# Kernel optimization log

Hardware: AMD Instinct MI355X
Metric: run time of the kernel (lower is better)

Reference implementation:

```python
import jax, jax.numpy as jnp
import numpy as np


def setup_inputs() -> dict:
    key = jax.random.key(0)
    k1, k2, k3 = jax.random.split(key, 3)
    V, B, T = 8192, 8, 1024
    x = jax.random.randint(k1, (B, T), 0, V, dtype=jnp.int64)
    y = jax.random.randint(k2, (B, T), 0, V, dtype=jnp.int64)
    emb = jax.random.normal(k3, (V, V), dtype=jnp.float32)
    return {"x": x, "y": y, "emb": emb}


def reference(x, y, emb):
    # token embedding lookup: [B, T, C] with C == vocab_size
    logits = emb[x]
    B, T, C = logits.shape
    # Causal mean pooling. softmax over a tril(ones) mask assigns uniform
    # weight 1/(t+1) to positions 0..t, i.e. a causal running mean.
    # Equivalent to the original's avg_matrix @ logits, computed in O(T*C).
    denom = jnp.arange(1, T + 1, dtype=logits.dtype)[:, None]  # [T, 1]
    logits_prev_mean = jnp.cumsum(logits, axis=1) / denom      # [B, T, C]
    # cross_entropy with mean reduction over B*T positions
    logp = jax.nn.log_softmax(logits_prev_mean, axis=-1)
    nll = -jnp.take_along_axis(logp, y[..., None], axis=-1)[..., 0]  # [B, T]
    loss = jnp.mean(nll)
    return logits, loss
```

## Files before the change

kernel.cpp:

```cpp
#include <hip/hip_runtime.h>

#define V 8192
#define B 8
#define T 1024
#define NSEG 16
#define SEGLEN 64
#define CSLICE 1024
#define NCHUNK 32
#define CHUNK 256

typedef float f32x4 __attribute__((ext_vector_type(4)));

__device__ __forceinline__ void nt_store4(float4* p, float4 v) {
    __builtin_nontemporal_store(*(f32x4*)&v, (f32x4*)p);
}

__global__ __launch_bounds__(256) void sum_kernel(
    const float* __restrict__ emb, const int* __restrict__ x,
    float* __restrict__ segsum)
{
    const int slice = blockIdx.x;
    const int seg   = blockIdx.y;
    const int b     = blockIdx.z;
    const int lane  = threadIdx.x & 63;
    const int c4    = (slice * CSLICE + threadIdx.x * 4) >> 2;

    const int xi = x[b * T + seg * SEGLEN + lane];

    const float4* emb4 = (const float4*)emb;
    float4 acc = make_float4(0.f, 0.f, 0.f, 0.f);
    float4 vbuf[4];
#pragma unroll
    for (int k = 0; k < 4; ++k)
        vbuf[k] = emb4[(size_t)__shfl(xi, k, 64) * (V / 4) + c4];

#pragma unroll
    for (int i = 0; i < SEGLEN; i += 4) {
#pragma unroll
        for (int k = 0; k < 4; ++k) {
            float4 cur = vbuf[k];
            const int nxt = i + 4 + k;
            if (nxt < SEGLEN)
                vbuf[k] = emb4[(size_t)__shfl(xi, nxt, 64) * (V / 4) + c4];
            acc.x += cur.x; acc.y += cur.y; acc.z += cur.z; acc.w += cur.w;
        }
    }
    ((float4*)segsum)[(size_t)(b * NSEG + seg) * (V / 4) + c4] = acc;
}

__global__ __launch_bounds__(256) void fused_kernel(
    const float* __restrict__ emb, const int* __restrict__ x,
    const int* __restrict__ y, const float* __restrict__ segsum,
    float* __restrict__ logits, float* __restrict__ P, float* __restrict__ tval)
{
    const int wave  = threadIdx.x >> 6;
    const int lane  = threadIdx.x & 63;
    const int chunk = blockIdx.x * 4 + wave;
    const int seg   = blockIdx.y;
    const int b     = blockIdx.z;
    const int c0    = chunk * CHUNK + lane * 4;
    const int c4    = c0 >> 2;
    const int tbase = seg * SEGLEN;

    const float4* ss4 = (const float4*)segsum;
    float4 S = make_float4(0.f, 0.f, 0.f, 0.f);
    for (int s = 0; s < seg; ++s) {
        float4 v = ss4[(size_t)(b * NSEG + s) * (V / 4) + c4];
        S.x += v.x; S.y += v.y; S.z += v.z; S.w += v.w;
    }

    const int   xi   = x[b * T + tbase + lane];
    const int   yi   = y[b * T + tbase + lane];
    const float invi = 1.0f / (float)(tbase + lane + 1);

    const float4* emb4    = (const float4*)emb;
    float4*       logits4 = (float4*)logits;

    float4 vbuf[4];
#pragma unroll
    for (int k = 0; k < 4; ++k)
        vbuf[k] = emb4[(size_t)__shfl(xi, k, 64) * (V / 4) + c4];

    float myP = 0.f;
    for (int i = 0; i < SEGLEN; i += 4) {
#pragma unroll
        for (int k = 0; k < 4; ++k) {
            const int ii  = i + k;
            float4 cur = vbuf[k];
            const int nxt = ii + 4;
            if (nxt < SEGLEN)
                vbuf[k] = emb4[(size_t)__shfl(xi, nxt, 64) * (V / 4) + c4];

            const int t   = tbase + ii;
            const int pos = b * T + t;
            nt_store4(&logits4[(size_t)pos * (V / 4) + c4], cur);
            S.x += cur.x; S.y += cur.y; S.z += cur.z; S.w += cur.w;
            const float inv = __shfl(invi, ii, 64);
            const float m0 = S.x * inv, m1 = S.y * inv, m2 = S.z * inv, m3 = S.w * inv;
            float e = __expf(m0) + __expf(m1) + __expf(m2) + __expf(m3);

            const int yc = __shfl(yi, ii, 64);
            const unsigned d = (unsigned)(yc - c0);
            if (d < 4u) {
                const float mv = (d == 0) ? m0 : (d == 1) ? m1 : (d == 2) ? m2 : m3;
                tval[pos] = mv;
            }
#pragma unroll
            for (int off = 32; off; off >>= 1) e += __shfl_xor(e, off, 64);
            if (lane == ii) myP = e;
        }
    }
    P[(size_t)chunk * (B * T) + b * T + tbase + lane] = myP;
}

__global__ __launch_bounds__(256) void loss_kernel(
    const float* __restrict__ P, const float* __restrict__ tval,
    float* __restrict__ loss)
{
    const int pos = blockIdx.x * 256 + threadIdx.x;
    float s = 0.f;
#pragma unroll
    for (int ch = 0; ch < NCHUNK; ++ch) s += P[(size_t)ch * (B * T) + pos];
    float nll = __logf(s) - tval[pos];

#pragma unroll
    for (int off = 32; off; off >>= 1) nll += __shfl_xor(nll, off, 64);
    __shared__ float red[4];
    const int wid = threadIdx.x >> 6;
    if ((threadIdx.x & 63) == 0) red[wid] = nll;
    __syncthreads();
    if (threadIdx.x == 0) {
        const float tot = red[0] + red[1] + red[2] + red[3];
        atomicAdd(loss, tot * (1.0f / (float)(B * T)));
    }
}

extern "C" void kernel_launch(void* const* d_in, const int* in_sizes, int n_in,
                              void* d_out, int out_size, void* d_ws, size_t ws_size,
                              hipStream_t stream) {
    const int*   x   = (const int*)d_in[0];
    const int*   y   = (const int*)d_in[1];
    const float* emb = (const float*)d_in[2];

    float* logits = (float*)d_out;
    float* loss   = logits + (size_t)B * T * V;

    float* segsum = (float*)d_ws;
    float* P      = segsum + (size_t)B * NSEG * V;
    float* tval   = P + (size_t)NCHUNK * B * T;

    hipMemsetAsync(loss, 0, sizeof(float), stream);
    sum_kernel<<<dim3(V / CSLICE, NSEG, B), 256, 0, stream>>>(emb, x, segsum);
    fused_kernel<<<dim3(NCHUNK / 4, NSEG, B), 256, 0, stream>>>(emb, x, y, segsum, logits, P, tval);
    loss_kernel<<<dim3(B * T / 256), 256, 0, stream>>>(P, tval, loss);
}
```

Measured before the change: 468.0 us.

## Halve segment length and precompute segment prefix sums in a separate kernel

Segments shrink from 64 to 32 tokens, doubling the grid of both the segment-sum and fused kernels so more blocks run in parallel with shorter serial chains. A new prefix kernel computes an exclusive scan over the segment sums once, so each fused block reads a single prefix vector instead of summing up to all earlier segments. This adds an extra launch and extra workspace traffic for the prefix array. Lanes are now masked to the segment length, so half of each wave's lanes hold duplicate indices.

Result: no change. 471.2 us (+0.7%).

```diff
diff --git a/kernel.cpp b/kernel.cpp
--- a/kernel.cpp
+++ b/kernel.cpp
@@ -3,8 +3,8 @@
 #define V 8192
 #define B 8
 #define T 1024
-#define NSEG 16
-#define SEGLEN 64
+#define NSEG 32
+#define SEGLEN 32
 #define CSLICE 1024
 #define NCHUNK 32
 #define CHUNK 256
@@ -25,7 +25,7 @@
     const int lane  = threadIdx.x & 63;
     const int c4    = (slice * CSLICE + threadIdx.x * 4) >> 2;
 
-    const int xi = x[b * T + seg * SEGLEN + lane];
+    const int xi = x[b * T + seg * SEGLEN + (lane & (SEGLEN - 1))];
 
     const float4* emb4 = (const float4*)emb;
     float4 acc = make_float4(0.f, 0.f, 0.f, 0.f);
@@ -48,9 +48,26 @@
     ((float4*)segsum)[(size_t)(b * NSEG + seg) * (V / 4) + c4] = acc;
 }
 
+__global__ __launch_bounds__(64) void prefix_kernel(
+    const float* __restrict__ segsum, float* __restrict__ segpre)
+{
+    const int g  = blockIdx.x * 64 + threadIdx.x;
+    const int b  = g / (V / 4);
+    const int c4 = g % (V / 4);
+    const float4* ss4 = (const float4*)segsum;
+    float4*       sp4 = (float4*)segpre;
+    float4 run = make_float4(0.f, 0.f, 0.f, 0.f);
+#pragma unroll 4
+    for (int s = 0; s < NSEG; ++s) {
+        sp4[(size_t)(b * NSEG + s) * (V / 4) + c4] = run;
+        float4 v = ss4[(size_t)(b * NSEG + s) * (V / 4) + c4];
+        run.x += v.x; run.y += v.y; run.z += v.z; run.w += v.w;
+    }
+}
+
 __global__ __launch_bounds__(256) void fused_kernel(
     const float* __restrict__ emb, const int* __restrict__ x,
-    const int* __restrict__ y, const float* __restrict__ segsum,
+    const int* __restrict__ y, const float* __restrict__ segpre,
     float* __restrict__ logits, float* __restrict__ P, float* __restrict__ tval)
 {
     const int wave  = threadIdx.x >> 6;
@@ -62,16 +79,12 @@
     const int c4    = c0 >> 2;
     const int tbase = seg * SEGLEN;
 
-    const float4* ss4 = (const float4*)segsum;
-    float4 S = make_float4(0.f, 0.f, 0.f, 0.f);
-    for (int s = 0; s < seg; ++s) {
-        float4 v = ss4[(size_t)(b * NSEG + s) * (V / 4) + c4];
-        S.x += v.x; S.y += v.y; S.z += v.z; S.w += v.w;
-    }
+    const float4* sp4 = (const float4*)segpre;
+    float4 S = sp4[(size_t)(b * NSEG + seg) * (V / 4) + c4];
 
-    const int   xi   = x[b * T + tbase + lane];
-    const int   yi   = y[b * T + tbase + lane];
-    const float invi = 1.0f / (float)(tbase + lane + 1);
+    const int   xi   = x[b * T + tbase + (lane & (SEGLEN - 1))];
+    const int   yi   = y[b * T + tbase + (lane & (SEGLEN - 1))];
+    const float invi = 1.0f / (float)(tbase + (lane & (SEGLEN - 1)) + 1);
 
     const float4* emb4    = (const float4*)emb;
     float4*       logits4 = (float4*)logits;
@@ -110,7 +123,8 @@
             if (lane == ii) myP = e;
         }
     }
-    P[(size_t)chunk * (B * T) + b * T + tbase + lane] = myP;
+    if (lane < SEGLEN)
+        P[(size_t)chunk * (B * T) + b * T + tbase + lane] = myP;
 }
 
 __global__ __launch_bounds__(256) void loss_kernel(
@@ -146,11 +160,13 @@
     float* loss   = logits + (size_t)B * T * V;
 
     float* segsum = (float*)d_ws;
-    float* P      = segsum + (size_t)B * NSEG * V;
+    float* segpre = segsum + (size_t)B * NSEG * V;
+    float* P      = segpre + (size_t)B * NSEG * V;
     float* tval   = P + (size_t)NCHUNK * B * T;
 
     hipMemsetAsync(loss, 0, sizeof(float), stream);
     sum_kernel<<<dim3(V / CSLICE, NSEG, B), 256, 0, stream>>>(emb, x, segsum);
-    fused_kernel<<<dim3(NCHUNK / 4, NSEG, B), 256, 0, stream>>>(emb, x, y, segsum, logits, P, tval);
+    prefix_kernel<<<dim3(B * (V / 4) / 64), 64, 0, stream>>>(segsum, segpre);
+    fused_kernel<<<dim3(NCHUNK / 4, NSEG, B), 256, 0, stream>>>(emb, x, y, segpre, logits, P, tval);
     loss_kernel<<<dim3(B * T / 256), 256, 0, stream>>>(P, tval, loss);
 }
```
